# Kernel tuning notes

Measured on AMD Instinct MI355X. Metric: run time of the kernel, lower is better.

## Reference

```python
import jax, jax.numpy as jnp
import numpy as np
from jax import lax


def _shifted(X, k, alpha):
    # alpha * roll(X, -k, 0) + (1 - alpha) * roll(X, -k-1, 0), via gather
    N = X.shape[0]
    idx = (jnp.arange(N) + k) % N
    return alpha * X[idx] + (1.0 - alpha) * X[(idx + 1) % N]


def _all_distances(D_q, D_p, steps):
    # steps: [S] float32 signed step values. Returns [S] mean L2 distances.
    N = D_q.shape[0]
    rows = jnp.arange(N)

    def dist_one(step):
        s = jnp.abs(step)
        k = jnp.floor(s).astype(jnp.int32)          # int(step) of |step|
        alpha = s - k.astype(step.dtype)
        diff = lax.cond(
            step >= 0,
            lambda: _shifted(D_q, k, alpha) - D_p,   # shift query forward
            lambda: D_q - _shifted(D_p, k, alpha),   # shift positive (ref) forward
        )
        norms = jnp.sqrt(jnp.sum(diff * diff, axis=-1))  # [N]
        valid = rows < (N - k)                       # rows [:N - int_step]
        return jnp.sum(jnp.where(valid, norms, 0.0)) / (N - k).astype(norms.dtype)

    def body(carry, step):
        return carry, dist_one(step)

    _, dists = lax.scan(body, None, steps)
    return dists


def setup_inputs() -> dict:
    key = jax.random.key(0)
    k1, k2 = jax.random.split(key)
    N, D = 100000, 256
    return {
        "D_q": jax.random.normal(k1, (N, D), dtype=jnp.float32),
        "D_p": jax.random.normal(k2, (N, D), dtype=jnp.float32),
        "max_step": 60,
        "step_size": 1,
    }


def reference(D_q, D_p, max_step, step_size):
    # Same candidate step schedule as the torch loop (static, built on host).
    steps_np = np.concatenate([
        np.arange(0, max_step, step_size),
        -np.arange(1, max_step + 1, step_size),
    ]).astype(np.float32)
    steps = jnp.asarray(steps_np)                    # [2*max_step/step_size]
    dists = _all_distances(D_q, D_p, steps)
    i = jnp.argmin(dists)
    return steps[i], dists[i]
```

## Files before the change

### kernel.cpp

```cpp
#include <hip/hip_runtime.h>
#include <math.h>


typedef __attribute__((ext_vector_type(8))) __bf16 bf16x8;
typedef __attribute__((ext_vector_type(16))) float f32x16;
typedef __attribute__((ext_vector_type(8))) unsigned short us8;

#define LDSH 280
#define RING 6
#define MAXS 128
#define NREP 32

__device__ __forceinline__ unsigned short f2bf(float x) {
  return __builtin_bit_cast(unsigned short, (__bf16)x);
}

__global__ __launch_bounds__(576, 1)
void band_kernel(const float* __restrict__ Q, const float* __restrict__ P,
                 double* __restrict__ ws,
                 const int* __restrict__ msp, const int* __restrict__ ssp,
                 int N, int TS, int nsb, int gridB) {
  __shared__ __align__(16) unsigned short Bsh[RING * 32 * LDSH];
  __shared__ __align__(16) unsigned short Qsh[2 * 32 * LDSH];
  __shared__ float NpS[RING * 32];
  __shared__ float NqS[2 * 32];
  __shared__ float sums[MAXS];
  __shared__ float red[12];
  __shared__ int packs[2];

  const int t = threadIdx.x;
  const int lane = t & 63;
  const int wid = t >> 6;
  const int ms = msp[0], ss = ssp[0];
  const int S1 = (ms + ss - 1) / ss;
  const int S = 2 * S1;

  if (blockIdx.x >= gridB) {
    const int si = blockIdx.x - gridB;
    if (si >= S) return;
    int k, qr, pr;
    if (si < S1) { k = si * ss;            qr = 0;           pr = N - (k + 1); }
    else         { k = 1 + (si - S1) * ss; qr = N - (k + 1); pr = 0; }
    float sq = 0.f;
    if (t < 256) {
      const float e = Q[(size_t)qr * 256 + t] - P[(size_t)pr * 256 + t];
      sq = e * e;
    }
    #pragma unroll
    for (int off = 32; off >= 1; off >>= 1) sq += __shfl_xor(sq, off);
    if (lane == 0) red[wid] = sq;
    __syncthreads();
    if (t == 0) {
      float tot = 0.f;
      #pragma unroll
      for (int w = 0; w < 9; ++w) tot += red[w];
      ws[(size_t)NREP * MAXS + si] = (double)sqrtf(tot);
    }
    return;
  }

  const int T0 = blockIdx.x * nsb;
  int ns = TS - T0; if (ns > nsb) ns = nsb;
  if (ns <= 0) return;

  for (int i = t; i < MAXS; i += 576) sums[i] = 0.f;
  if (t == 0) { packs[0] = 0; packs[1] = 0; }
  __syncthreads();

  volatile int* vprod = &packs[0];
  volatile int* vcons = &packs[1];

  if (wid >= 5) {
    const int pw = wid - 5;
    const int rr = pw * 8 + (lane >> 3);
    const int li = lane & 7;

    float4 vp[8], vq[8];

    auto issueT = [&](const float* __restrict__ base, int tau, float4* v) {
      const int gr = tau * 32 + rr;
      if (gr >= 0 && gr < N) {
        const float* src = base + (size_t)gr * 256 + li * 8;
        #pragma unroll
        for (int j = 0; j < 4; ++j) {
          v[2 * j]     = *reinterpret_cast<const float4*>(src + j * 64);
          v[2 * j + 1] = *reinterpret_cast<const float4*>(src + j * 64 + 4);
        }
      } else {
        #pragma unroll
        for (int j = 0; j < 8; ++j) v[j] = make_float4(0.f, 0.f, 0.f, 0.f);
      }
    };

    auto commitT = [&](unsigned short* dst, float* ndst, int slot, const float4* v) {
      float nrm = 0.f;
      unsigned short* row = dst + slot * 32 * LDSH + rr * LDSH + li * 8;
      #pragma unroll
      for (int j = 0; j < 4; ++j) {
        const float f0 = v[2*j].x, f1 = v[2*j].y, f2 = v[2*j].z, f3 = v[2*j].w;
        const float f4 = v[2*j+1].x, f5 = v[2*j+1].y, f6 = v[2*j+1].z, f7 = v[2*j+1].w;
        nrm = fmaf(f0, f0, nrm); nrm = fmaf(f1, f1, nrm);
        nrm = fmaf(f2, f2, nrm); nrm = fmaf(f3, f3, nrm);
        nrm = fmaf(f4, f4, nrm); nrm = fmaf(f5, f5, nrm);
        nrm = fmaf(f6, f6, nrm); nrm = fmaf(f7, f7, nrm);
        us8 h;
        h[0] = f2bf(f0); h[1] = f2bf(f1); h[2] = f2bf(f2); h[3] = f2bf(f3);
        h[4] = f2bf(f4); h[5] = f2bf(f5); h[6] = f2bf(f6); h[7] = f2bf(f7);
        *reinterpret_cast<us8*>(row + j * 64) = h;
      }
      nrm += __shfl_xor(nrm, 1);
      nrm += __shfl_xor(nrm, 2);
      nrm += __shfl_xor(nrm, 4);
      if (li == 0) ndst[slot * 32 + rr] = nrm;
    };

    #pragma unroll 1
    for (int r = -4; r < ns; ++r) {
      const int tauP = T0 + r + 2;
      const bool doQ = (r >= 0);
      issueT(P, tauP, vp);
      if (doQ) issueT(Q, T0 + r, vq);
      const int needc = r - 1;
      if (needc > 0) {
        for (;;) {
          const int v = *vcons;
          if ((v & 63) >= needc && ((v >> 6) & 63) >= needc &&
              ((v >> 12) & 63) >= needc && ((v >> 18) & 63) >= needc &&
              ((v >> 24) & 63) >= needc) break;
          __builtin_amdgcn_s_sleep(2);
        }
      }
      commitT(Bsh, NpS, (tauP + 12) % RING, vp);
      if (doQ) commitT(Qsh, NqS, (T0 + r) & 1, vq);
      __threadfence_block();
      if (lane == 0) atomicAdd(&packs[0], 1 << (8 * pw));
    }
  } else {
    const int l31 = lane & 31;
    const int hi = lane >> 5;

    int slotR[16];
    #pragma unroll
    for (int r = 0; r < 16; ++r) {
      const int arow = (r & 3) + 8 * (r >> 2) + 4 * hi;
      const int d = arow - l31 - (wid - 2) * 32;
      int slot = -1;
      if (d >= 1) {
        const int k = d - 1;
        if (k < ms && (k % ss) == 0) slot = k / ss;
      } else if (d <= -2) {
        const int kk = -d - 1;
        if (kk <= ms && ((kk - 1) % ss) == 0) slot = S1 + (kk - 1) / ss;
      }
      if (slot >= MAXS) slot = -1;
      slotR[r] = slot;
    }
    float racc[16];
    #pragma unroll
    for (int r = 0; r < 16; ++r) racc[r] = 0.f;

    #pragma unroll 1
    for (int s = 0; s < ns; ++s) {
      const int T = T0 + s;
      const int need = s + 5;
      for (;;) {
        const int v = *vprod;
        if ((v & 255) >= need && ((v >> 8) & 255) >= need &&
            ((v >> 16) & 255) >= need && ((v >> 24) & 255) >= need) break;
        __builtin_amdgcn_s_sleep(2);
      }
      __threadfence_block();

      const int tauW = T - 2 + wid;
      const int slot6 = (tauW + 12) % RING;
      const unsigned short* Ab = &Qsh[(T & 1) * 32 * LDSH + l31 * LDSH + hi * 8];
      const unsigned short* Bb = &Bsh[slot6 * 32 * LDSH + l31 * LDSH + hi * 8];
      f32x16 acc0 = {}, acc1 = {};
      __builtin_amdgcn_s_setprio(1);
      #pragma unroll
      for (int ks = 0; ks < 16; ks += 2) {
        const bf16x8 a0 = *reinterpret_cast<const bf16x8*>(Ab + ks * 16);
        const bf16x8 b0 = *reinterpret_cast<const bf16x8*>(Bb + ks * 16);
        const bf16x8 a1 = *reinterpret_cast<const bf16x8*>(Ab + ks * 16 + 16);
        const bf16x8 b1 = *reinterpret_cast<const bf16x8*>(Bb + ks * 16 + 16);
        acc0 = __builtin_amdgcn_mfma_f32_32x32x16_bf16(a0, b0, acc0, 0, 0, 0);
        acc1 = __builtin_amdgcn_mfma_f32_32x32x16_bf16(a1, b1, acc1, 0, 0, 0);
      }
      __builtin_amdgcn_s_setprio(0);

      const int bcol = tauW * 32 + l31;
      if (bcol >= 0 && bcol < N) {
        const float npW = NpS[slot6 * 32 + l31];
        const int aT = T * 32;
        #pragma unroll
        for (int r = 0; r < 16; ++r) {
          const int arow = (r & 3) + 8 * (r >> 2) + 4 * hi;
          if (slotR[r] >= 0 && (aT + arow) < N) {
            const float n2 = NqS[(T & 1) * 32 + arow] + npW
                             - 2.0f * (acc0[r] + acc1[r]);
            racc[r] += sqrtf(fmaxf(n2, 0.f));
          }
        }
      }

      __threadfence_block();
      if (lane == 0) atomicAdd(&packs[1], 1 << (6 * wid));
    }

    #pragma unroll
    for (int r = 0; r < 16; ++r)
      if (slotR[r] >= 0 && racc[r] != 0.f) atomicAdd(&sums[slotR[r]], racc[r]);
  }

  __syncthreads();
  if (t < S && t < MAXS) {
    const float v = sums[t];
    if (v != 0.f)
      unsafeAtomicAdd(&ws[(size_t)(blockIdx.x & (NREP - 1)) * MAXS + t], (double)v);
  }
}

__global__ void finalize_kernel(const double* __restrict__ ws, float* __restrict__ out,
                                const int* __restrict__ msp, const int* __restrict__ ssp,
                                int N) {
  __shared__ double dist_sh[MAXS];
  const int t = threadIdx.x;
  const int ms = msp[0], ss = ssp[0];
  const int S1 = (ms + ss - 1) / ss;
  const int S = 2 * S1;
  if (t < S && t < MAXS) {
    double tot = 0.0;
    for (int rep = 0; rep < NREP; ++rep) tot += ws[(size_t)rep * MAXS + t];
    tot += ws[(size_t)NREP * MAXS + t];
    const int k = (t < S1) ? t * ss : 1 + (t - S1) * ss;
    dist_sh[t] = tot / (double)(N - k);
  }
  __syncthreads();
  if (t == 0) {
    int best = 0;
    double bd = dist_sh[0];
    for (int s = 1; s < S && s < MAXS; ++s)
      if (dist_sh[s] < bd) { bd = dist_sh[s]; best = s; }
    const int k = (best < S1) ? best * ss : 1 + (best - S1) * ss;
    out[0] = (best < S1) ? (float)k : -(float)k;
    out[1] = (float)bd;
  }
}

extern "C" void kernel_launch(void* const* d_in, const int* in_sizes, int n_in,
                              void* d_out, int out_size, void* d_ws, size_t ws_size,
                              hipStream_t stream) {
  const float* Q   = (const float*)d_in[0];
  const float* P   = (const float*)d_in[1];
  const int*   msp = (const int*)d_in[2];
  const int*   ssp = (const int*)d_in[3];
  const int N = in_sizes[0] / 256;
  double* ws = (double*)d_ws;

  hipMemsetAsync(d_ws, 0, (size_t)(NREP + 1) * MAXS * sizeof(double), stream);

  const int TS = (N + 31) / 32;
  int nsb = (TS + 249) / 250;
  if (nsb < 1) nsb = 1;
  if (nsb > 60) nsb = 60;
  const int gridB = (TS + nsb - 1) / nsb;

  band_kernel<<<gridB + MAXS, 576, 0, stream>>>(Q, P, ws, msp, ssp,
                                                N, TS, nsb, gridB);
  finalize_kernel<<<1, 128, 0, stream>>>(ws, (float*)d_out, msp, ssp, N);
}
```

Before: 61.87 us.

## Batch prologue P-tile loads, swizzle blocks across XCDs, shorten spin sleeps

The producer warps now issue all four prologue P-tile global loads up front and then commit them one by one, rather than loading and committing each tile serially. This is meant to overlap load latency during pipeline fill. Block indices are remapped so that consecutive strips land on the same XCD, improving L2 locality for the shared halo rows. Spin-wait sleep durations drop from 2 to 1 on both the producer and consumer sides to reduce wake-up latency. The cost is higher register pressure from the four prologue buffers and more polling traffic on LDS.

```diff
diff --git a/kernel.cpp b/kernel.cpp
--- a/kernel.cpp
+++ b/kernel.cpp
@@ -13,6 +13,12 @@
 
 __device__ __forceinline__ unsigned short f2bf(float x) {
   return __builtin_bit_cast(unsigned short, (__bf16)x);
+}
+
+__device__ __forceinline__ int xcd_swz(int bid, int nwg) {
+  const int q = nwg >> 3, r = nwg & 7;
+  const int x = bid & 7, i = bid >> 3;
+  return (x < r ? x * (q + 1) : r * (q + 1) + (x - r) * q) + i;
 }
 
 __global__ __launch_bounds__(576, 1)
@@ -59,7 +65,8 @@
     return;
   }
 
-  const int T0 = blockIdx.x * nsb;
+  const int sb = xcd_swz(blockIdx.x, gridB);
+  const int T0 = sb * nsb;
   int ns = TS - T0; if (ns > nsb) ns = nsb;
   if (ns <= 0) return;
 
@@ -74,8 +81,6 @@
     const int pw = wid - 5;
     const int rr = pw * 8 + (lane >> 3);
     const int li = lane & 7;
-
-    float4 vp[8], vq[8];
 
     auto issueT = [&](const float* __restrict__ base, int tau, float4* v) {
       const int gr = tau * 32 + rr;
@@ -114,12 +119,32 @@
       if (li == 0) ndst[slot * 32 + rr] = nrm;
     };
 
+    {
+      float4 w0[8], w1[8], w2[8], w3[8];
+      issueT(P, T0 - 2, w0);
+      issueT(P, T0 - 1, w1);
+      issueT(P, T0,     w2);
+      issueT(P, T0 + 1, w3);
+      commitT(Bsh, NpS, (T0 + 10) % RING, w0);
+      __threadfence_block();
+      if (lane == 0) atomicAdd(&packs[0], 1 << (8 * pw));
+      commitT(Bsh, NpS, (T0 + 11) % RING, w1);
+      __threadfence_block();
+      if (lane == 0) atomicAdd(&packs[0], 1 << (8 * pw));
+      commitT(Bsh, NpS, (T0 + 12) % RING, w2);
+      __threadfence_block();
+      if (lane == 0) atomicAdd(&packs[0], 1 << (8 * pw));
+      commitT(Bsh, NpS, (T0 + 13) % RING, w3);
+      __threadfence_block();
+      if (lane == 0) atomicAdd(&packs[0], 1 << (8 * pw));
+    }
+
+    float4 vp[8], vq[8];
     #pragma unroll 1
-    for (int r = -4; r < ns; ++r) {
+    for (int r = 0; r < ns; ++r) {
       const int tauP = T0 + r + 2;
-      const bool doQ = (r >= 0);
       issueT(P, tauP, vp);
-      if (doQ) issueT(Q, T0 + r, vq);
+      issueT(Q, T0 + r, vq);
       const int needc = r - 1;
       if (needc > 0) {
         for (;;) {
@@ -127,11 +152,11 @@
           if ((v & 63) >= needc && ((v >> 6) & 63) >= needc &&
               ((v >> 12) & 63) >= needc && ((v >> 18) & 63) >= needc &&
               ((v >> 24) & 63) >= needc) break;
-          __builtin_amdgcn_s_sleep(2);
+          __builtin_amdgcn_s_sleep(1);
         }
       }
       commitT(Bsh, NpS, (tauP + 12) % RING, vp);
-      if (doQ) commitT(Qsh, NqS, (T0 + r) & 1, vq);
+      commitT(Qsh, NqS, (T0 + r) & 1, vq);
       __threadfence_block();
       if (lane == 0) atomicAdd(&packs[0], 1 << (8 * pw));
     }
@@ -167,7 +192,7 @@
         const int v = *vprod;
         if ((v & 255) >= need && ((v >> 8) & 255) >= need &&
             ((v >> 16) & 255) >= need && ((v >> 24) & 255) >= need) break;
-        __builtin_amdgcn_s_sleep(2);
+        __builtin_amdgcn_s_sleep(1);
       }
       __threadfence_block();
 
```

Measured after the change: 62.39 us. Within noise of the previous version (+0.8%).

## Double-buffer producer global loads and replace fences with LDS waitcnt

Applied to the files above, without the earlier changes.

Producer warps now hold two register sets and issue the global loads for tile j+2 right after committing tile j, so loads overlap with waiting and LDS commits instead of being serialized. Block-level thread fences are replaced by an explicit lgkmcnt wait plus sched barriers, sleep intervals are shortened, and ring slots are indexed relative to the block start. Blocks are also remapped with an XCD-aware swizzle so contiguous tiles share an XCD's L2. The extra register sets raise VGPR pressure, and the weaker fence depends on LDS ordering being enough for the producer-consumer counters.

```diff
diff --git a/kernel.cpp b/kernel.cpp
--- a/kernel.cpp
+++ b/kernel.cpp
@@ -7,12 +7,25 @@
 typedef __attribute__((ext_vector_type(8))) unsigned short us8;
 
 #define LDSH 280
-#define RING 6
+#define PR 6
 #define MAXS 128
 #define NREP 32
 
+#define LGKM_FENCE()                                                          \
+  do {                                                                        \
+    __builtin_amdgcn_sched_barrier(0);                                        \
+    asm volatile("s_waitcnt lgkmcnt(0)" ::: "memory");                        \
+    __builtin_amdgcn_sched_barrier(0);                                        \
+  } while (0)
+
 __device__ __forceinline__ unsigned short f2bf(float x) {
   return __builtin_bit_cast(unsigned short, (__bf16)x);
+}
+
+__device__ __forceinline__ int xcd_swz(int bid, int nwg) {
+  const int q = nwg >> 3, r = nwg & 7;
+  const int x = bid & 7, i = bid >> 3;
+  return (x < r ? x * (q + 1) : r * (q + 1) + (x - r) * q) + i;
 }
 
 __global__ __launch_bounds__(576, 1)
@@ -20,9 +33,9 @@
                  double* __restrict__ ws,
                  const int* __restrict__ msp, const int* __restrict__ ssp,
                  int N, int TS, int nsb, int gridB) {
-  __shared__ __align__(16) unsigned short Bsh[RING * 32 * LDSH];
+  __shared__ __align__(16) unsigned short Bsh[PR * 32 * LDSH];
   __shared__ __align__(16) unsigned short Qsh[2 * 32 * LDSH];
-  __shared__ float NpS[RING * 32];
+  __shared__ float NpS[PR * 32];
   __shared__ float NqS[2 * 32];
   __shared__ float sums[MAXS];
   __shared__ float red[12];
@@ -59,7 +72,8 @@
     return;
   }
 
-  const int T0 = blockIdx.x * nsb;
+  const int sb = xcd_swz(blockIdx.x, gridB);
+  const int T0 = sb * nsb;
   int ns = TS - T0; if (ns > nsb) ns = nsb;
   if (ns <= 0) return;
 
@@ -74,8 +88,6 @@
     const int pw = wid - 5;
     const int rr = pw * 8 + (lane >> 3);
     const int li = lane & 7;
-
-    float4 vp[8], vq[8];
 
     auto issueT = [&](const float* __restrict__ base, int tau, float4* v) {
       const int gr = tau * 32 + rr;
@@ -114,27 +126,43 @@
       if (li == 0) ndst[slot * 32 + rr] = nrm;
     };
 
-    #pragma unroll 1
-    for (int r = -4; r < ns; ++r) {
-      const int tauP = T0 + r + 2;
-      const bool doQ = (r >= 0);
-      issueT(P, tauP, vp);
-      if (doQ) issueT(Q, T0 + r, vq);
-      const int needc = r - 1;
-      if (needc > 0) {
-        for (;;) {
-          const int v = *vcons;
-          if ((v & 63) >= needc && ((v >> 6) & 63) >= needc &&
-              ((v >> 12) & 63) >= needc && ((v >> 18) & 63) >= needc &&
-              ((v >> 24) & 63) >= needc) break;
-          __builtin_amdgcn_s_sleep(2);
-        }
-      }
-      commitT(Bsh, NpS, (tauP + 12) % RING, vp);
-      if (doQ) commitT(Qsh, NqS, (T0 + r) & 1, vq);
-      __threadfence_block();
-      if (lane == 0) atomicAdd(&packs[0], 1 << (8 * pw));
-    }
+    float4 Ap[8], Aq[8], Bp[8], Bq[8];
+    const int JT = ns + 4;
+
+#define P_ISSUE(JJ, SET)                                                      \
+    { const int pj_ = (JJ);                                                   \
+      if (pj_ < JT) {                                                         \
+        issueT(P, T0 + pj_ - 2, SET##p);                                      \
+        if (pj_ >= 4) issueT(Q, T0 + pj_ - 4, SET##q);                        \
+      } }
+#define P_STEP(JJ, SET)                                                       \
+    { const int j_ = (JJ);                                                    \
+      const int needc = j_ - 5;                                               \
+      if (needc > 0) {                                                        \
+        for (;;) {                                                            \
+          const int v = *vcons;                                               \
+          if ((v & 63) >= needc && ((v >> 6) & 63) >= needc &&                \
+              ((v >> 12) & 63) >= needc && ((v >> 18) & 63) >= needc &&       \
+              ((v >> 24) & 63) >= needc) break;                               \
+          __builtin_amdgcn_s_sleep(1);                                        \
+        }                                                                     \
+      }                                                                       \
+      commitT(Bsh, NpS, j_ % PR, SET##p);                                     \
+      if (j_ >= 4) commitT(Qsh, NqS, (j_ - 4) & 1, SET##q);                   \
+      LGKM_FENCE();                                                           \
+      if (lane == 0) atomicAdd(&packs[0], 1 << (8 * pw));                     \
+      P_ISSUE(j_ + 2, SET); }
+
+    P_ISSUE(0, A);
+    P_ISSUE(1, B);
+    int j = 0;
+    for (; j + 2 <= JT; j += 2) {
+      P_STEP(j, A);
+      P_STEP(j + 1, B);
+    }
+    if (j < JT) P_STEP(j, A);
+#undef P_STEP
+#undef P_ISSUE
   } else {
     const int l31 = lane & 31;
     const int hi = lane >> 5;
@@ -167,14 +195,15 @@
         const int v = *vprod;
         if ((v & 255) >= need && ((v >> 8) & 255) >= need &&
             ((v >> 16) & 255) >= need && ((v >> 24) & 255) >= need) break;
-        __builtin_amdgcn_s_sleep(2);
-      }
-      __threadfence_block();
+        __builtin_amdgcn_s_sleep(1);
+      }
+      __builtin_amdgcn_sched_barrier(0);
 
       const int tauW = T - 2 + wid;
-      const int slot6 = (tauW + 12) % RING;
-      const unsigned short* Ab = &Qsh[(T & 1) * 32 * LDSH + l31 * LDSH + hi * 8];
-      const unsigned short* Bb = &Bsh[slot6 * 32 * LDSH + l31 * LDSH + hi * 8];
+      const int slotP = (s + wid) % PR;
+      const int slotQ = s & 1;
+      const unsigned short* Ab = &Qsh[slotQ * 32 * LDSH + l31 * LDSH + hi * 8];
+      const unsigned short* Bb = &Bsh[slotP * 32 * LDSH + l31 * LDSH + hi * 8];
       f32x16 acc0 = {}, acc1 = {};
       __builtin_amdgcn_s_setprio(1);
       #pragma unroll
@@ -190,20 +219,20 @@
 
       const int bcol = tauW * 32 + l31;
       if (bcol >= 0 && bcol < N) {
-        const float npW = NpS[slot6 * 32 + l31];
+        const float npW = NpS[slotP * 32 + l31];
         const int aT = T * 32;
         #pragma unroll
         for (int r = 0; r < 16; ++r) {
           const int arow = (r & 3) + 8 * (r >> 2) + 4 * hi;
           if (slotR[r] >= 0 && (aT + arow) < N) {
-            const float n2 = NqS[(T & 1) * 32 + arow] + npW
+            const float n2 = NqS[slotQ * 32 + arow] + npW
                              - 2.0f * (acc0[r] + acc1[r]);
             racc[r] += sqrtf(fmaxf(n2, 0.f));
           }
         }
       }
 
-      __threadfence_block();
+      LGKM_FENCE();
       if (lane == 0) atomicAdd(&packs[1], 1 << (6 * wid));
     }
 
@@ -262,7 +291,7 @@
   const int TS = (N + 31) / 32;
   int nsb = (TS + 249) / 250;
   if (nsb < 1) nsb = 1;
-  if (nsb > 60) nsb = 60;
+  if (nsb > 59) nsb = 59;
   const int gridB = (TS + nsb - 1) / nsb;
 
   band_kernel<<<gridB + MAXS, 576, 0, stream>>>(Q, P, ws, msp, ssp,
```

Measured after the change: 64.54 us. 1.04x slower.
